# Optimization experiments

Measured on AMD Instinct MI355X. Metric: run time of the kernel, lower is better.

## Reference

```python
import jax, jax.numpy as jnp
import numpy as np

D, DK, DV = 1024, 128, 128
N = 8192


def setup_inputs() -> dict:
    key = jax.random.key(0)
    ks = jax.random.split(key, 7)
    s = 1.0 / np.sqrt(D)
    return {
        "X": jax.random.normal(ks[0], (N, D), dtype=jnp.float32),
        "Wq": jax.random.uniform(ks[1], (D, DK), jnp.float32, -s, s),
        "bq": jax.random.uniform(ks[2], (DK,), jnp.float32, -s, s),
        "Wk": jax.random.uniform(ks[3], (D, DK), jnp.float32, -s, s),
        "bk": jax.random.uniform(ks[4], (DK,), jnp.float32, -s, s),
        "Wv": jax.random.uniform(ks[5], (D, DV), jnp.float32, -s, s),
        "bv": jax.random.uniform(ks[6], (DV,), jnp.float32, -s, s),
    }


def reference(X, Wq, bq, Wk, bk, Wv, bv):
    # Projections (torch Linear: y = x @ W^T + b; here W stored as [in, out])
    Q = X @ Wq + bq            # [N, d_k]
    K = X @ Wk + bk            # [N, d_k]
    V = X @ Wv + bv            # [N, d_v]
    n, d_k = Q.shape
    scores = (Q @ K.T) / jnp.sqrt(jnp.asarray(d_k, Q.dtype))  # [N, N]
    # Causal mask: positions j > i get -inf before softmax
    causal = jnp.tril(jnp.ones((n, n), dtype=bool))
    scores = jnp.where(causal, scores, -jnp.inf)
    weights = jax.nn.softmax(scores, axis=-1)  # [N, N]
    return weights @ V          # [N, d_v]
```

## Files before the change

kernel.cpp:

```cpp
#include <hip/hip_runtime.h>
#include <hip/hip_bf16.h>

#define N_TOK 8192
#define D_IN  1024
#define DK    128
#define NT    256

typedef __attribute__((ext_vector_type(8))) short short8;
typedef __attribute__((ext_vector_type(4))) float f32x4;

static __device__ __forceinline__ unsigned short f2bf(float f) {
    __hip_bfloat16 h = __float2bfloat16(f);
    return __builtin_bit_cast(unsigned short, h);
}

static __device__ __forceinline__ void gl_lds16(const void* g, void* l) {
    __builtin_amdgcn_global_load_lds(
        (const __attribute__((address_space(1))) void*)g,
        (__attribute__((address_space(3))) void*)l, 16, 0, 0);
}

__global__ __launch_bounds__(256) void wtrans_kernel(
    const float* __restrict__ Wq, const float* __restrict__ Wk,
    const float* __restrict__ Wv, unsigned short* __restrict__ Wt)
{
    __shared__ unsigned short T[64][72];
    const int proj = blockIdx.y;
    const float* W = (proj == 0) ? Wq : (proj == 1) ? Wk : Wv;
    unsigned short* out = Wt + (size_t)proj * DK * D_IN;
    const int k0 = (blockIdx.x & 15) * 64, n0 = (blockIdx.x >> 4) * 64;
    const int tid = threadIdx.x;
    #pragma unroll
    for (int i = 0; i < 4; i++) {
        int e = tid + i * 256;
        int r = e >> 4, c4 = e & 15;
        float4 v = *reinterpret_cast<const float4*>(&W[(size_t)(k0 + r) * DK + n0 + c4 * 4]);
        T[c4 * 4 + 0][r] = f2bf(v.x);
        T[c4 * 4 + 1][r] = f2bf(v.y);
        T[c4 * 4 + 2][r] = f2bf(v.z);
        T[c4 * 4 + 3][r] = f2bf(v.w);
    }
    __syncthreads();
    #pragma unroll
    for (int i = 0; i < 4; i++) {
        int e = tid + i * 256;
        int r = e >> 4, c4 = e & 15;
        *reinterpret_cast<ushort4*>(&out[(size_t)(n0 + r) * D_IN + k0 + c4 * 4]) =
            *reinterpret_cast<const ushort4*>(&T[r][c4 * 4]);
    }
}

__global__ __launch_bounds__(256) void proj_kernel(
    const float* __restrict__ X, const unsigned short* __restrict__ Wt,
    const float* __restrict__ bq, const float* __restrict__ bk,
    const float* __restrict__ bv,
    unsigned short* __restrict__ Qb, unsigned short* __restrict__ Kb,
    unsigned short* __restrict__ Vt)
{
    __shared__ unsigned short As[64][72];

    const int tid  = threadIdx.x;
    const int wid  = tid >> 6, lane = tid & 63;
    const int g    = lane >> 4, r16 = lane & 15;
    const int wm   = wid >> 1, wn = wid & 1;
    const int mb   = blockIdx.x * 64;
    const int proj = blockIdx.y;

    const unsigned short* Wtp = Wt + (size_t)proj * DK * D_IN;
    const float* bias = (proj == 0) ? bq : (proj == 1) ? bk : bv;

    f32x4 acc[2][4] = {};

    for (int k0 = 0; k0 < D_IN; k0 += 64) {
        #pragma unroll
        for (int i = 0; i < 4; i++) {
            int e = tid + i * 256;
            int r = e >> 4, c4 = e & 15;
            const float4 v = *reinterpret_cast<const float4*>(
                &X[(size_t)(mb + r) * D_IN + k0 + c4 * 4]);
            ushort4 h;
            h.x = f2bf(v.x); h.y = f2bf(v.y); h.z = f2bf(v.z); h.w = f2bf(v.w);
            *reinterpret_cast<ushort4*>(&As[r][c4 * 4]) = h;
        }
        __syncthreads();
        #pragma unroll
        for (int kk = 0; kk < 64; kk += 32) {
            short8 af[2], bfr[4];
            #pragma unroll
            for (int mi = 0; mi < 2; mi++)
                af[mi] = *reinterpret_cast<const short8*>(&As[wm * 32 + mi * 16 + r16][kk + g * 8]);
            #pragma unroll
            for (int ni = 0; ni < 4; ni++)
                bfr[ni] = *reinterpret_cast<const short8*>(
                    &Wtp[(size_t)(wn * 64 + ni * 16 + r16) * D_IN + k0 + kk + g * 8]);
            #pragma unroll
            for (int mi = 0; mi < 2; mi++)
                #pragma unroll
                for (int ni = 0; ni < 4; ni++)
                    acc[mi][ni] = __builtin_amdgcn_mfma_f32_16x16x32_bf16(
                        af[mi], bfr[ni], acc[mi][ni], 0, 0, 0);
        }
        __syncthreads();
    }

    if (proj < 2) {
        unsigned short* out = (proj == 0) ? Qb : Kb;
        #pragma unroll
        for (int ni = 0; ni < 4; ni++) {
            int n = wn * 64 + ni * 16 + r16;
            float b = bias[n];
            #pragma unroll
            for (int mi = 0; mi < 2; mi++) {
                #pragma unroll
                for (int e = 0; e < 4; e++) {
                    int m = mb + wm * 32 + mi * 16 + g * 4 + e;
                    int nc = n;
                    if (proj == 1)
                        nc = ((((n >> 3) ^ (m & 7)) << 3) | (n & 7));
                    out[(size_t)m * DK + nc] = f2bf(acc[mi][ni][e] + b);
                }
            }
        }
    } else {
        #pragma unroll
        for (int ni = 0; ni < 4; ni++) {
            int n = wn * 64 + ni * 16 + r16;
            float b = bias[n];
            #pragma unroll
            for (int mi = 0; mi < 2; mi++) {
                int m0 = mb + wm * 32 + mi * 16 + g * 4;
                int mblk = (((m0 & 31) >> 3) ^ (n & 3));
                int mp = (m0 & ~31) | (mblk << 3) | (m0 & 7);
                ushort4 h;
                h.x = f2bf(acc[mi][ni][0] + b);
                h.y = f2bf(acc[mi][ni][1] + b);
                h.z = f2bf(acc[mi][ni][2] + b);
                h.w = f2bf(acc[mi][ni][3] + b);
                *reinterpret_cast<ushort4*>(&Vt[(size_t)n * N_TOK + mp]) = h;
            }
        }
    }
}

__global__ __launch_bounds__(256, 3) void attn_partial(
    const unsigned short* __restrict__ Qb, const unsigned short* __restrict__ Ksw,
    const unsigned short* __restrict__ Vsw,
    float* __restrict__ Opart, float* __restrict__ Mpart, float* __restrict__ Lpart,
    float* __restrict__ O, int chunk_tiles, int max_chunks, int direct)
{
    __shared__ unsigned short Klds[2][32][128];
    __shared__ unsigned short Vlds[2][128][32];
    __shared__ unsigned short Pq[4][32][36];

    const int qb = blockIdx.x, c = blockIdx.y;
    const int j0 = c * chunk_tiles;
    const int jmax = 4 * qb + 4;
    const int jend = min(j0 + chunk_tiles, jmax);
    if (j0 >= jend) return;
    const int nt = jend - j0;

    const int tid = threadIdx.x;
    const int wid = tid >> 6, lane = tid & 63;
    const int g = lane >> 4, r16 = lane & 15;
    const int t = qb * 4 + wid;
    const int qw = t * 32;
    const float scale2 = 0.08838834764831845f * 1.4426950408889634f;

    auto STAGE = [&](int buf, int kvb) {
        #pragma unroll
        for (int s = 0; s < 2; s++) {
            int ob = ((wid * 2 + s) << 10);
            gl_lds16((const char*)Ksw + ((size_t)kvb << 8) + ob + (lane << 4),
                     (char*)&Klds[buf][0][0] + ob);
        }
        #pragma unroll
        for (int s = 0; s < 2; s++) {
            int ob = ((wid * 2 + s) << 10);
            int o = ob + (lane << 4);
            int d = o >> 6, cb = o & 63;
            gl_lds16((const char*)Vsw + (((size_t)d * N_TOK + kvb) << 1) + cb,
                     (char*)&Vlds[buf][0][0] + ob);
        }
    };

    short8 qf[2][4];
    #pragma unroll
    for (int mi = 0; mi < 2; mi++)
        #pragma unroll
        for (int kd = 0; kd < 4; kd++)
            qf[mi][kd] = *reinterpret_cast<const short8*>(
                &Qb[(size_t)(qw + mi * 16 + r16) * DK + kd * 32 + g * 8]);

    f32x4 o_acc[2][8] = {};
    float m_run[2] = {-1e30f, -1e30f}, l_run[2] = {0.f, 0.f};

    STAGE(0, j0 * 32);
    __syncthreads();

    int cur = 0;
    for (int it = 0; it < nt; ++it) {
        const int kvb = (j0 + it) * 32;
        if (it + 1 < nt) STAGE(cur ^ 1, kvb + 32);

        const unsigned short* Kl = &Klds[cur][0][0];
        const unsigned short* Vl = &Vlds[cur][0][0];

        f32x4 st[2][2] = {};
        #pragma unroll
        for (int kd = 0; kd < 4; kd++) {
            int swb = ((((kd << 2) | g) ^ (r16 & 7)) << 3);
            short8 kf0 = *reinterpret_cast<const short8*>(Kl + r16 * 128 + swb);
            short8 kf1 = *reinterpret_cast<const short8*>(Kl + (16 + r16) * 128 + swb);
            st[0][0] = __builtin_amdgcn_mfma_f32_16x16x32_bf16(kf0, qf[0][kd], st[0][0], 0, 0, 0);
            st[0][1] = __builtin_amdgcn_mfma_f32_16x16x32_bf16(kf0, qf[1][kd], st[0][1], 0, 0, 0);
            st[1][0] = __builtin_amdgcn_mfma_f32_16x16x32_bf16(kf1, qf[0][kd], st[1][0], 0, 0, 0);
            st[1][1] = __builtin_amdgcn_mfma_f32_16x16x32_bf16(kf1, qf[1][kd], st[1][1], 0, 0, 0);
        }

        const bool anymask = (kvb + 31 > qw);
        float alpha[2];
        #pragma unroll
        for (int mi = 0; mi < 2; mi++) {
            const int qrow = qw + mi * 16 + r16;
            float s[2][4];
            #pragma unroll
            for (int ni = 0; ni < 2; ni++)
                #pragma unroll
                for (int e = 0; e < 4; e++) {
                    float v = st[ni][mi][e] * scale2;
                    if (anymask && (kvb + ni * 16 + g * 4 + e > qrow)) v = -1e30f;
                    s[ni][e] = v;
                }
            float lm = fmaxf(fmaxf(fmaxf(s[0][0], s[0][1]), fmaxf(s[0][2], s[0][3])),
                             fmaxf(fmaxf(s[1][0], s[1][1]), fmaxf(s[1][2], s[1][3])));
            lm = fmaxf(lm, __shfl_xor(lm, 16));
            lm = fmaxf(lm, __shfl_xor(lm, 32));
            float mnew = fmaxf(m_run[mi], lm);
            alpha[mi] = exp2f(m_run[mi] - mnew);
            float ps[2][4], ls;
            #pragma unroll
            for (int ni = 0; ni < 2; ni++)
                #pragma unroll
                for (int e = 0; e < 4; e++)
                    ps[ni][e] = exp2f(s[ni][e] - mnew);
            ls = ((ps[0][0] + ps[0][1]) + (ps[0][2] + ps[0][3]))
               + ((ps[1][0] + ps[1][1]) + (ps[1][2] + ps[1][3]));
            ls += __shfl_xor(ls, 16);
            ls += __shfl_xor(ls, 32);
            l_run[mi] = l_run[mi] * alpha[mi] + ls;
            m_run[mi] = mnew;
            #pragma unroll
            for (int ni = 0; ni < 2; ni++) {
                ushort4 pk;
                pk.x = f2bf(ps[ni][0]); pk.y = f2bf(ps[ni][1]);
                pk.z = f2bf(ps[ni][2]); pk.w = f2bf(ps[ni][3]);
                *reinterpret_cast<ushort4*>(&Pq[wid][mi * 16 + r16][ni * 16 + g * 4]) = pk;
            }
        }
        if (__any(alpha[0] < 1.f) || __any(alpha[1] < 1.f)) {
            #pragma unroll
            for (int mi = 0; mi < 2; mi++)
                #pragma unroll
                for (int df = 0; df < 8; df++)
                    #pragma unroll
                    for (int e = 0; e < 4; e++)
                        o_acc[mi][df][e] *= alpha[mi];
        }
        short8 pb0 = *reinterpret_cast<const short8*>(&Pq[wid][r16][g * 8]);
        short8 pb1 = *reinterpret_cast<const short8*>(&Pq[wid][16 + r16][g * 8]);
        const int swv = ((g ^ (r16 & 3)) << 3);
        #pragma unroll
        for (int df = 0; df < 8; df++) {
            short8 vf = *reinterpret_cast<const short8*>(Vl + (df * 16 + r16) * 32 + swv);
            o_acc[0][df] = __builtin_amdgcn_mfma_f32_16x16x32_bf16(vf, pb0, o_acc[0][df], 0, 0, 0);
            o_acc[1][df] = __builtin_amdgcn_mfma_f32_16x16x32_bf16(vf, pb1, o_acc[1][df], 0, 0, 0);
        }

        __syncthreads();
        cur ^= 1;
    }

    if (direct) {
        #pragma unroll
        for (int mi = 0; mi < 2; mi++) {
            float inv = 1.0f / l_run[mi];
            #pragma unroll
            for (int df = 0; df < 8; df++) {
                f32x4 r = o_acc[mi][df];
                r[0] *= inv; r[1] *= inv; r[2] *= inv; r[3] *= inv;
                *reinterpret_cast<f32x4*>(
                    &O[(size_t)(qw + mi * 16 + r16) * DK + df * 16 + g * 4]) = r;
            }
        }
    } else {
        size_t pb0i = ((size_t)t * max_chunks + c) * 32;
        #pragma unroll
        for (int mi = 0; mi < 2; mi++) {
            #pragma unroll
            for (int df = 0; df < 8; df++)
                *reinterpret_cast<f32x4*>(
                    &Opart[(pb0i + mi * 16 + r16) * 128 + df * 16 + g * 4]) = o_acc[mi][df];
            if (g == 0) {
                Mpart[pb0i + mi * 16 + r16] = m_run[mi];
                Lpart[pb0i + mi * 16 + r16] = l_run[mi];
            }
        }
    }
}

__global__ __launch_bounds__(256) void attn_merge(
    const float* __restrict__ Opart, const float* __restrict__ Mpart,
    const float* __restrict__ Lpart, float* __restrict__ O,
    int chunk_tiles, int max_chunks)
{
    __shared__ float Ms[32], Ls[32], Fs[16][32];
    const int t = blockIdx.x;
    const int nc = t / chunk_tiles + 1;
    const int tid = threadIdx.x;

    if (tid < 32) {
        float M = -1e30f;
        for (int c = 0; c < nc; c++)
            M = fmaxf(M, Mpart[((size_t)t * max_chunks + c) * 32 + tid]);
        float L = 0.f;
        for (int c = 0; c < nc; c++) {
            size_t pb = ((size_t)t * max_chunks + c) * 32 + tid;
            L += exp2f(Mpart[pb] - M) * Lpart[pb];
        }
        Ms[tid] = M; Ls[tid] = L;
    }
    __syncthreads();
    for (int cc = tid >> 5; cc < nc; cc += 8) {
        int row = tid & 31;
        Fs[cc][row] = exp2f(Mpart[((size_t)t * max_chunks + cc) * 32 + row] - Ms[row]);
    }
    __syncthreads();
    #pragma unroll
    for (int it = 0; it < 4; it++) {
        int idx = tid + it * 256;
        int row = idx >> 5, c4 = idx & 31;
        float4 acc = {0.f, 0.f, 0.f, 0.f};
        for (int c = 0; c < nc; c++) {
            const float4 v = *reinterpret_cast<const float4*>(
                &Opart[(((size_t)t * max_chunks + c) * 32 + row) * 128 + c4 * 4]);
            float f = Fs[c][row];
            acc.x += f * v.x; acc.y += f * v.y; acc.z += f * v.z; acc.w += f * v.w;
        }
        float inv = 1.0f / Ls[row];
        float4 r;
        r.x = acc.x * inv; r.y = acc.y * inv; r.z = acc.z * inv; r.w = acc.w * inv;
        *reinterpret_cast<float4*>(&O[((size_t)t * 32 + row) * DK + c4 * 4]) = r;
    }
}

extern "C" void kernel_launch(void* const* d_in, const int* in_sizes, int n_in,
                              void* d_out, int out_size, void* d_ws, size_t ws_size,
                              hipStream_t stream) {
    const float* X  = (const float*)d_in[0];
    const float* Wq = (const float*)d_in[1];
    const float* bq = (const float*)d_in[2];
    const float* Wk = (const float*)d_in[3];
    const float* bk = (const float*)d_in[4];
    const float* Wv = (const float*)d_in[5];
    const float* bv = (const float*)d_in[6];
    float* O = (float*)d_out;

    unsigned short* Qb = (unsigned short*)d_ws;
    unsigned short* Kb = Qb + (size_t)N_TOK * DK;
    unsigned short* Vt = Kb + (size_t)N_TOK * DK;
    unsigned short* Wt = Vt + (size_t)N_TOK * DK;
    float* Opart = (float*)(Wt + (size_t)3 * DK * D_IN);
    size_t base_bytes = (size_t)((char*)Opart - (char*)d_ws);

    int chunk_tiles = 0, max_chunks = 1, direct = 0;
    const int opts[4] = {16, 32, 64, 128};
    for (int i = 0; i < 4; i++) {
        int ct = opts[i], mc = NT / ct;
        size_t need = base_bytes + (size_t)NT * mc * 32 * (128 + 2) * sizeof(float);
        if (need <= ws_size) { chunk_tiles = ct; max_chunks = mc; break; }
    }
    if (!chunk_tiles) { chunk_tiles = NT; max_chunks = 1; direct = 1; }
    float* Mpart = Opart + (size_t)NT * max_chunks * 32 * 128;
    float* Lpart = Mpart + (size_t)NT * max_chunks * 32;

    wtrans_kernel<<<dim3(32, 3), 256, 0, stream>>>(Wq, Wk, Wv, Wt);
    proj_kernel<<<dim3(128, 3), 256, 0, stream>>>(X, Wt, bq, bk, bv, Qb, Kb, Vt);
    int grid_c = direct ? 1 : max_chunks;
    attn_partial<<<dim3(64, grid_c), 256, 0, stream>>>(
        Qb, Kb, Vt, Opart, Mpart, Lpart, O, chunk_tiles, max_chunks, direct);
    if (!direct)
        attn_merge<<<dim3(NT), 256, 0, stream>>>(Opart, Mpart, Lpart, O,
                                                 chunk_tiles, max_chunks);
}
```

Baseline: 116.7 us.

## Fuse QKV projections into one kernel and pipeline attention staging waits

The projection kernel now computes Q, K and V together in one block over 32 rows, so each X tile is read and converted once instead of three times. The X tile is prefetched into registers and double-buffered in LDS. In the attention loop, the full syncthreads is replaced by an explicit vmcnt wait plus a raw barrier so the next K/V prefetch can stay in flight. MFMA sections are wrapped in s_setprio to favour matrix issue. The vmcnt(4) count assumes a fixed number of outstanding loads per stage, which is fragile if the staging code changes.

```diff
diff --git a/kernel.cpp b/kernel.cpp
--- a/kernel.cpp
+++ b/kernel.cpp
@@ -50,85 +50,99 @@
     }
 }
 
-__global__ __launch_bounds__(256) void proj_kernel(
+__global__ __launch_bounds__(256) void proj_fused(
     const float* __restrict__ X, const unsigned short* __restrict__ Wt,
     const float* __restrict__ bq, const float* __restrict__ bk,
     const float* __restrict__ bv,
     unsigned short* __restrict__ Qb, unsigned short* __restrict__ Kb,
     unsigned short* __restrict__ Vt)
 {
-    __shared__ unsigned short As[64][72];
-
-    const int tid  = threadIdx.x;
-    const int wid  = tid >> 6, lane = tid & 63;
-    const int g    = lane >> 4, r16 = lane & 15;
-    const int wm   = wid >> 1, wn = wid & 1;
-    const int mb   = blockIdx.x * 64;
-    const int proj = blockIdx.y;
-
-    const unsigned short* Wtp = Wt + (size_t)proj * DK * D_IN;
-    const float* bias = (proj == 0) ? bq : (proj == 1) ? bk : bv;
-
-    f32x4 acc[2][4] = {};
-
-    for (int k0 = 0; k0 < D_IN; k0 += 64) {
-        #pragma unroll
-        for (int i = 0; i < 4; i++) {
+    __shared__ unsigned short Xs[2][32][72];
+
+    const int tid = threadIdx.x;
+    const int wid = tid >> 6, lane = tid & 63;
+    const int g = lane >> 4, r16 = lane & 15;
+    const int mb = blockIdx.x * 32;
+
+    float4 xr[2];
+    auto XLOAD = [&](int k0) {
+        #pragma unroll
+        for (int i = 0; i < 2; i++) {
             int e = tid + i * 256;
             int r = e >> 4, c4 = e & 15;
-            const float4 v = *reinterpret_cast<const float4*>(
+            xr[i] = *reinterpret_cast<const float4*>(
                 &X[(size_t)(mb + r) * D_IN + k0 + c4 * 4]);
+        }
+    };
+    auto XWRITE = [&](int buf) {
+        #pragma unroll
+        for (int i = 0; i < 2; i++) {
+            int e = tid + i * 256;
+            int r = e >> 4, c4 = e & 15;
             ushort4 h;
-            h.x = f2bf(v.x); h.y = f2bf(v.y); h.z = f2bf(v.z); h.w = f2bf(v.w);
-            *reinterpret_cast<ushort4*>(&As[r][c4 * 4]) = h;
-        }
-        __syncthreads();
+            h.x = f2bf(xr[i].x); h.y = f2bf(xr[i].y);
+            h.z = f2bf(xr[i].z); h.w = f2bf(xr[i].w);
+            *reinterpret_cast<ushort4*>(&Xs[buf][r][c4 * 4]) = h;
+        }
+    };
+
+    f32x4 acc[2][6] = {};
+
+    XLOAD(0); XWRITE(0);
+    __syncthreads();
+    for (int s = 0; s < 16; ++s) {
+        const int k0 = s * 64;
+        const int cur = s & 1;
+        if (s + 1 < 16) XLOAD(k0 + 64);
         #pragma unroll
         for (int kk = 0; kk < 64; kk += 32) {
-            short8 af[2], bfr[4];
+            short8 af[2], bfr[6];
             #pragma unroll
             for (int mi = 0; mi < 2; mi++)
-                af[mi] = *reinterpret_cast<const short8*>(&As[wm * 32 + mi * 16 + r16][kk + g * 8]);
-            #pragma unroll
-            for (int ni = 0; ni < 4; ni++)
+                af[mi] = *reinterpret_cast<const short8*>(&Xs[cur][mi * 16 + r16][kk + g * 8]);
+            #pragma unroll
+            for (int ni = 0; ni < 6; ni++) {
+                int nn = wid * 96 + ni * 16;
+                int pj = nn >> 7;
                 bfr[ni] = *reinterpret_cast<const short8*>(
-                    &Wtp[(size_t)(wn * 64 + ni * 16 + r16) * D_IN + k0 + kk + g * 8]);
+                    &Wt[((size_t)pj * DK + (nn & 127) + r16) * D_IN + k0 + kk + g * 8]);
+            }
+            __builtin_amdgcn_s_setprio(1);
             #pragma unroll
             for (int mi = 0; mi < 2; mi++)
                 #pragma unroll
-                for (int ni = 0; ni < 4; ni++)
+                for (int ni = 0; ni < 6; ni++)
                     acc[mi][ni] = __builtin_amdgcn_mfma_f32_16x16x32_bf16(
                         af[mi], bfr[ni], acc[mi][ni], 0, 0, 0);
-        }
+            __builtin_amdgcn_s_setprio(0);
+        }
+        if (s + 1 < 16) XWRITE((s + 1) & 1);
         __syncthreads();
     }
 
-    if (proj < 2) {
-        unsigned short* out = (proj == 0) ? Qb : Kb;
-        #pragma unroll
-        for (int ni = 0; ni < 4; ni++) {
-            int n = wn * 64 + ni * 16 + r16;
-            float b = bias[n];
-            #pragma unroll
-            for (int mi = 0; mi < 2; mi++) {
+    #pragma unroll
+    for (int ni = 0; ni < 6; ni++) {
+        int nn = wid * 96 + ni * 16;
+        int pj = nn >> 7;
+        int n = (nn & 127) + r16;
+        const float* bias = (pj == 0) ? bq : (pj == 1) ? bk : bv;
+        float b = bias[n];
+        if (pj < 2) {
+            unsigned short* out = (pj == 0) ? Qb : Kb;
+            #pragma unroll
+            for (int mi = 0; mi < 2; mi++)
                 #pragma unroll
                 for (int e = 0; e < 4; e++) {
-                    int m = mb + wm * 32 + mi * 16 + g * 4 + e;
+                    int m = mb + mi * 16 + g * 4 + e;
                     int nc = n;
-                    if (proj == 1)
+                    if (pj == 1)
                         nc = ((((n >> 3) ^ (m & 7)) << 3) | (n & 7));
                     out[(size_t)m * DK + nc] = f2bf(acc[mi][ni][e] + b);
                 }
-            }
-        }
-    } else {
-        #pragma unroll
-        for (int ni = 0; ni < 4; ni++) {
-            int n = wn * 64 + ni * 16 + r16;
-            float b = bias[n];
+        } else {
             #pragma unroll
             for (int mi = 0; mi < 2; mi++) {
-                int m0 = mb + wm * 32 + mi * 16 + g * 4;
+                int m0 = mb + mi * 16 + g * 4;
                 int mblk = (((m0 & 31) >> 3) ^ (n & 3));
                 int mp = (m0 & ~31) | (mblk << 3) | (m0 & 7);
                 ushort4 h;
@@ -195,12 +209,19 @@
     float m_run[2] = {-1e30f, -1e30f}, l_run[2] = {0.f, 0.f};
 
     STAGE(0, j0 * 32);
-    __syncthreads();
 
     int cur = 0;
     for (int it = 0; it < nt; ++it) {
         const int kvb = (j0 + it) * 32;
-        if (it + 1 < nt) STAGE(cur ^ 1, kvb + 32);
+        if (it + 1 < nt) {
+            STAGE(cur ^ 1, kvb + 32);
+            asm volatile("s_waitcnt vmcnt(4)" ::: "memory");
+        } else {
+            asm volatile("s_waitcnt vmcnt(0)" ::: "memory");
+        }
+        __builtin_amdgcn_sched_barrier(0);
+        __builtin_amdgcn_s_barrier();
+        __builtin_amdgcn_sched_barrier(0);
 
         const unsigned short* Kl = &Klds[cur][0][0];
         const unsigned short* Vl = &Vlds[cur][0][0];
@@ -211,10 +232,12 @@
             int swb = ((((kd << 2) | g) ^ (r16 & 7)) << 3);
             short8 kf0 = *reinterpret_cast<const short8*>(Kl + r16 * 128 + swb);
             short8 kf1 = *reinterpret_cast<const short8*>(Kl + (16 + r16) * 128 + swb);
+            __builtin_amdgcn_s_setprio(1);
             st[0][0] = __builtin_amdgcn_mfma_f32_16x16x32_bf16(kf0, qf[0][kd], st[0][0], 0, 0, 0);
             st[0][1] = __builtin_amdgcn_mfma_f32_16x16x32_bf16(kf0, qf[1][kd], st[0][1], 0, 0, 0);
             st[1][0] = __builtin_amdgcn_mfma_f32_16x16x32_bf16(kf1, qf[0][kd], st[1][0], 0, 0, 0);
             st[1][1] = __builtin_amdgcn_mfma_f32_16x16x32_bf16(kf1, qf[1][kd], st[1][1], 0, 0, 0);
+            __builtin_amdgcn_s_setprio(0);
         }
 
         const bool anymask = (kvb + 31 > qw);
@@ -272,11 +295,15 @@
         #pragma unroll
         for (int df = 0; df < 8; df++) {
             short8 vf = *reinterpret_cast<const short8*>(Vl + (df * 16 + r16) * 32 + swv);
+            __builtin_amdgcn_s_setprio(1);
             o_acc[0][df] = __builtin_amdgcn_mfma_f32_16x16x32_bf16(vf, pb0, o_acc[0][df], 0, 0, 0);
             o_acc[1][df] = __builtin_amdgcn_mfma_f32_16x16x32_bf16(vf, pb1, o_acc[1][df], 0, 0, 0);
-        }
-
-        __syncthreads();
+            __builtin_amdgcn_s_setprio(0);
+        }
+
+        __builtin_amdgcn_sched_barrier(0);
+        __builtin_amdgcn_s_barrier();
+        __builtin_amdgcn_sched_barrier(0);
         cur ^= 1;
     }
 
@@ -384,7 +411,7 @@
     float* Lpart = Mpart + (size_t)NT * max_chunks * 32;
 
     wtrans_kernel<<<dim3(32, 3), 256, 0, stream>>>(Wq, Wk, Wv, Wt);
-    proj_kernel<<<dim3(128, 3), 256, 0, stream>>>(X, Wt, bq, bk, bv, Qb, Kb, Vt);
+    proj_fused<<<dim3(256), 256, 0, stream>>>(X, Wt, bq, bk, bv, Qb, Kb, Vt);
     int grid_c = direct ? 1 : max_chunks;
     attn_partial<<<dim3(64, grid_c), 256, 0, stream>>>(
         Qb, Kb, Vt, Opart, Mpart, Lpart, O, chunk_tiles, max_chunks, direct);
```

After: 112.4 us. 3.7% less time.
